# Kernel optimization log

Hardware: AMD Instinct MI355X
Metric: run time of the kernel (lower is better)

Reference implementation:

```python
import jax, jax.numpy as jnp
import numpy as np

BASE_T = 0.07
ALPHA = 0.5
EPS = 1e-12  # torch F.normalize eps


def _l2_normalize(x):
    norm = jnp.linalg.norm(x, axis=1, keepdims=True)
    return x / jnp.maximum(norm, EPS)


def setup_inputs() -> dict:
    key = jax.random.key(0)
    k1, k2, k3 = jax.random.split(key, 3)
    B, D, H, W = 4096, 512, 16, 16
    return {
        "emb1": jax.random.normal(k1, (B, D), dtype=jnp.float32),
        "emb2": jax.random.normal(k2, (B, D), dtype=jnp.float32),
        "attention_map": jax.random.uniform(k3, (B, H, W), dtype=jnp.float32),
    }


def reference(emb1, emb2, attention_map):
    B = emb1.shape[0]
    e1 = _l2_normalize(emb1)
    e2 = _l2_normalize(emb2)

    att = attention_map.mean(axis=(1, 2))                     # [B]
    temp = (BASE_T * (1.0 + ALPHA * att))[:, None]            # [B, 1]

    x = jnp.concatenate([e1, e2], axis=0)                     # [2B, D]
    x_swap = jnp.concatenate([e2, e1], axis=0)                # [2B, D]
    temp_cat = jnp.concatenate([temp, temp], axis=0)          # [2B, 1]

    sim = jnp.matmul(x, x.T) / temp_cat                       # [2B, 2B]
    pos_sim = jnp.sum(x * x_swap, axis=1) / temp_cat[:, 0]    # [2B]

    diag = jnp.eye(2 * B, dtype=bool)
    sim = jnp.where(diag, -jnp.inf, sim)                      # exp(-inf) = 0

    denominator = jnp.exp(sim).sum(axis=1)                    # [2B]
    loss = -jnp.log(jnp.exp(pos_sim) / denominator)
    return loss.mean()
```

## Files before the change

### kernel.cpp

```cpp
#include <hip/hip_runtime.h>
#include <hip/hip_bf16.h>
#include <math.h>

#define B_ROWS 4096
#define D_DIM 512
#define TWO_B 8192
#define HW_N 256
#define BASE_T 0.07f
#define ALPHA_C 0.5f
#define LOG2E 1.44269504088896340736f

typedef float v4f __attribute__((ext_vector_type(4)));

__device__ __forceinline__ float fast_exp2(float x) {
#if __has_builtin(__builtin_amdgcn_exp2f)
    return __builtin_amdgcn_exp2f(x);
#else
    return exp2f(x);
#endif
}

__global__ __launch_bounds__(256) void prep_kernel(
    const float* __restrict__ emb1, const float* __restrict__ emb2,
    const float* __restrict__ att, unsigned short* __restrict__ X8,
    float* __restrict__ inv_temp, float* __restrict__ pos)
{
    const int b = blockIdx.x;
    const int t = threadIdx.x;
    const float2 a1 = ((const float2*)(emb1 + (size_t)b * D_DIM))[t];
    const float2 a2 = ((const float2*)(emb2 + (size_t)b * D_DIM))[t];
    float av = att[(size_t)b * HW_N + t];
    float s1  = a1.x * a1.x + a1.y * a1.y;
    float s2  = a2.x * a2.x + a2.y * a2.y;
    float s12 = a1.x * a2.x + a1.y * a2.y;
    #pragma unroll
    for (int m = 1; m < 64; m <<= 1) {
        s1  += __shfl_xor(s1, m, 64);
        s2  += __shfl_xor(s2, m, 64);
        s12 += __shfl_xor(s12, m, 64);
        av  += __shfl_xor(av, m, 64);
    }
    __shared__ float red[4][4];
    const int w = t >> 6, lane = t & 63;
    if (lane == 0) { red[w][0] = s1; red[w][1] = s2; red[w][2] = s12; red[w][3] = av; }
    __syncthreads();
    const float T1  = red[0][0] + red[1][0] + red[2][0] + red[3][0];
    const float T2  = red[0][1] + red[1][1] + red[2][1] + red[3][1];
    const float T12 = red[0][2] + red[1][2] + red[2][2] + red[3][2];
    const float Ta  = red[0][3] + red[1][3] + red[2][3] + red[3][3];
    const float i1 = 1.0f / fmaxf(sqrtf(T1), 1e-12f);
    const float i2 = 1.0f / fmaxf(sqrtf(T2), 1e-12f);
    const float it = 1.0f / (BASE_T * (1.0f + ALPHA_C * (Ta * (1.0f / 256.0f))));
    const int p1 = __builtin_amdgcn_cvt_pk_fp8_f32(a1.x * i1, a1.y * i1, 0, false);
    const int p2 = __builtin_amdgcn_cvt_pk_fp8_f32(a2.x * i2, a2.y * i2, 0, false);
    X8[(size_t)b * 256 + t]            = (unsigned short)(p1 & 0xffff);
    X8[(size_t)(b + B_ROWS) * 256 + t] = (unsigned short)(p2 & 0xffff);
    if (t == 0) {
        inv_temp[b] = it * LOG2E;
        inv_temp[b + B_ROWS] = it * LOG2E;
        pos[b] = (T12 * i1 * i2) * it;
    }
}

__device__ __forceinline__ void gload_lds16(const void* g, void* s) {
    __builtin_amdgcn_global_load_lds(
        (const __attribute__((address_space(1))) unsigned int*)g,
        (__attribute__((address_space(3))) unsigned int*)s,
        16, 0, 0);
}

__global__ __launch_bounds__(256) void gram_kernel(
    const unsigned char* __restrict__ X8,
    const float* __restrict__ inv_temp,
    float* __restrict__ partial)
{
    const int bid = (blockIdx.x & 7) * 260 + (blockIdx.x >> 3);
    int rb = (int)((129.0f - sqrtf(129.0f * 129.0f - 8.0f * (float)bid)) * 0.5f);
    rb = rb < 0 ? 0 : (rb > 63 ? 63 : rb);
    while (rb > 0 && (rb * (129 - rb)) / 2 > bid) rb--;
    while (rb < 63 && ((rb + 1) * (129 - (rb + 1))) / 2 <= bid) rb++;
    const int cb = rb + (bid - (rb * (129 - rb)) / 2);

    __shared__ unsigned char smA[2][16384];
    __shared__ unsigned char smB[2][16384];

    const int rowBase = rb * 128;
    const int colBase = cb * 128;

    const int tid  = threadIdx.x;
    const int w    = tid >> 6;
    const int lane = tid & 63;
    const int quad = lane >> 4;
    const int t    = lane & 15;
    const int wm   = w >> 1;
    const int wn   = w & 1;

    const int srow   = lane >> 3;
    const int schunk = lane & 7;

    const unsigned char* Arow0 = X8 + (size_t)rowBase * D_DIM;
    const unsigned char* Brow0 = X8 + (size_t)colBase * D_DIM;

    v4f acc[4][4];
    #pragma unroll
    for (int a = 0; a < 4; a++)
        #pragma unroll
        for (int b2 = 0; b2 < 4; b2++)
            acc[a][b2] = v4f{0.0f, 0.0f, 0.0f, 0.0f};

    #pragma unroll
    for (int j = 0; j < 4; j++) {
        const int g = w * 4 + j;
        const int r = g * 8 + srow;
        const int gc = schunk ^ (r & 7);
        gload_lds16(Arow0 + (size_t)r * D_DIM + gc * 16, &smA[0][g * 1024]);
        gload_lds16(Brow0 + (size_t)r * D_DIM + gc * 16, &smB[0][g * 1024]);
    }
    __syncthreads();

    #pragma unroll
    for (int p = 0; p < 4; p++) {
        const int cur = p & 1;
        const int nxt = cur ^ 1;

        if (p < 3) {
            const int kk = (p + 1) * 128;
            #pragma unroll
            for (int j = 0; j < 4; j++) {
                const int g = w * 4 + j;
                const int r = g * 8 + srow;
                const int gc = schunk ^ (r & 7);
                gload_lds16(Arow0 + (size_t)r * D_DIM + kk + gc * 16, &smA[nxt][g * 1024]);
                gload_lds16(Brow0 + (size_t)r * D_DIM + kk + gc * 16, &smB[nxt][g * 1024]);
            }
        }

        #pragma unroll
        for (int s = 0; s < 4; s++) {
            const int pu = (s * 2 + (quad >> 1)) ^ (t & 7);
            const int off = pu * 16 + (quad & 1) * 8;
            long aF[4], bF[4];
            #pragma unroll
            for (int mi = 0; mi < 4; mi++)
                aF[mi] = *(const long*)&smA[cur][(wm * 64 + mi * 16 + t) * 128 + off];
            #pragma unroll
            for (int ni = 0; ni < 4; ni++)
                bF[ni] = *(const long*)&smB[cur][(wn * 64 + ni * 16 + t) * 128 + off];
            #pragma unroll
            for (int mi = 0; mi < 4; mi++)
                #pragma unroll
                for (int ni = 0; ni < 4; ni++)
                    acc[mi][ni] = __builtin_amdgcn_mfma_f32_16x16x32_fp8_fp8(
                        aF[mi], bF[ni], acc[mi][ni], 0, 0, 0);
        }

        __syncthreads();
    }

    v4f itv[4];
    #pragma unroll
    for (int mi = 0; mi < 4; mi++)
        itv[mi] = *(const v4f*)&inv_temp[rowBase + wm * 64 + mi * 16 + quad * 4];

    float* prow = partial + (size_t)(cb * 2 + wn) * TWO_B;
    #pragma unroll
    for (int mi = 0; mi < 4; mi++) {
        #pragma unroll
        for (int r = 0; r < 4; r++) {
            const int i = rowBase + wm * 64 + mi * 16 + quad * 4 + r;
            const float it = itv[mi][r];
            float s = 0.0f;
            #pragma unroll
            for (int ni = 0; ni < 4; ni++) {
                const int j = colBase + wn * 64 + ni * 16 + t;
                const float v = fast_exp2(acc[mi][ni][r] * it);
                s += (i == j) ? 0.0f : v;
            }
            s += __shfl_xor(s, 1, 64);
            s += __shfl_xor(s, 2, 64);
            s += __shfl_xor(s, 4, 64);
            s += __shfl_xor(s, 8, 64);
            if (t == 0) prow[i] = s;
        }
    }

    if (rb != cb) {
        float itj[4];
        float cs[4] = {0.0f, 0.0f, 0.0f, 0.0f};
        #pragma unroll
        for (int ni = 0; ni < 4; ni++)
            itj[ni] = inv_temp[colBase + wn * 64 + ni * 16 + t];
        #pragma unroll
        for (int mi = 0; mi < 4; mi++)
            #pragma unroll
            for (int r = 0; r < 4; r++)
                #pragma unroll
                for (int ni = 0; ni < 4; ni++)
                    cs[ni] += fast_exp2(acc[mi][ni][r] * itj[ni]);
        float* pcol = partial + (size_t)(rb * 2 + wm) * TWO_B;
        #pragma unroll
        for (int ni = 0; ni < 4; ni++) {
            cs[ni] += __shfl_xor(cs[ni], 16, 64);
            cs[ni] += __shfl_xor(cs[ni], 32, 64);
            if (quad == 0) pcol[colBase + wn * 64 + ni * 16 + t] = cs[ni];
        }
    }
}

__global__ __launch_bounds__(256) void finish1(
    const float* __restrict__ partial, const float* __restrict__ pos,
    float* __restrict__ blockSums)
{
    const int i = blockIdx.x * 256 + threadIdx.x;
    float d = 0.0f;
    #pragma unroll 8
    for (int s = 0; s < 128; s++) d += partial[(size_t)s * TWO_B + i];
    float li = logf(d) - pos[i & (B_ROWS - 1)];
    #pragma unroll
    for (int m = 1; m < 64; m <<= 1) li += __shfl_xor(li, m, 64);
    __shared__ float red[4];
    const int w = threadIdx.x >> 6, lane = threadIdx.x & 63;
    if (lane == 0) red[w] = li;
    __syncthreads();
    if (threadIdx.x == 0) blockSums[blockIdx.x] = red[0] + red[1] + red[2] + red[3];
}

__global__ void finish2(const float* __restrict__ blockSums, float* __restrict__ out)
{
    const int lane = threadIdx.x;
    float v = (lane < 32) ? blockSums[lane] : 0.0f;
    #pragma unroll
    for (int m = 1; m < 64; m <<= 1) v += __shfl_xor(v, m, 64);
    if (lane == 0) out[0] = v * (1.0f / 8192.0f);
}

extern "C" void kernel_launch(void* const* d_in, const int* in_sizes, int n_in,
                              void* d_out, int out_size, void* d_ws, size_t ws_size,
                              hipStream_t stream) {
    const float* emb1 = (const float*)d_in[0];
    const float* emb2 = (const float*)d_in[1];
    const float* att  = (const float*)d_in[2];
    float* out = (float*)d_out;

    char* ws = (char*)d_ws;
    unsigned short* X8 = (unsigned short*)ws;
    float* inv_temp    = (float*)(ws + 4194304);
    float* pos         = (float*)(ws + 4194304 + 32768);
    float* partial     = (float*)(ws + 4194304 + 32768 + 16384);
    float* blockSums   = (float*)(ws + 4194304 + 32768 + 16384 + 4194304);

    prep_kernel<<<B_ROWS, 256, 0, stream>>>(emb1, emb2, att, X8, inv_temp, pos);
    gram_kernel<<<2080, 256, 0, stream>>>((const unsigned char*)X8, inv_temp, partial);
    finish1<<<TWO_B / 256, 256, 0, stream>>>(partial, pos, blockSums);
    finish2<<<1, 64, 0, stream>>>(blockSums, out);
}
```

Measured before the change: 132.0 us.

## Use scaled 16x16x128 FP8 MFMA and load A fragments directly from global

Replaces the 16x16x32 FP8 MFMA with the gfx950 scaled 16x16x128 f8f6f4 MFMA (unit scales), cutting instruction count per k-step. The A operand is no longer staged through LDS: each lane reads its 32-byte fragment straight from global memory. This halves shared memory use, and a launch bound of 3 waves is added to raise occupancy. In exchange, A reads depend on global/L2 latency without double buffering, and the trailing sync on the last iteration is dropped.

```diff
diff --git a/kernel.cpp b/kernel.cpp
--- a/kernel.cpp
+++ b/kernel.cpp
@@ -11,6 +11,8 @@
 #define LOG2E 1.44269504088896340736f
 
 typedef float v4f __attribute__((ext_vector_type(4)));
+typedef int   v4i __attribute__((ext_vector_type(4)));
+typedef int   v8i __attribute__((ext_vector_type(8)));
 
 __device__ __forceinline__ float fast_exp2(float x) {
 #if __has_builtin(__builtin_amdgcn_exp2f)
@@ -69,7 +71,7 @@
         16, 0, 0);
 }
 
-__global__ __launch_bounds__(256) void gram_kernel(
+__global__ __launch_bounds__(256, 3) void gram_kernel(
     const unsigned char* __restrict__ X8,
     const float* __restrict__ inv_temp,
     float* __restrict__ partial)
@@ -81,7 +83,6 @@
     while (rb < 63 && ((rb + 1) * (129 - (rb + 1))) / 2 <= bid) rb++;
     const int cb = rb + (bid - (rb * (129 - rb)) / 2);
 
-    __shared__ unsigned char smA[2][16384];
     __shared__ unsigned char smB[2][16384];
 
     const int rowBase = rb * 128;
@@ -95,8 +96,8 @@
     const int wm   = w >> 1;
     const int wn   = w & 1;
 
-    const int srow   = lane >> 3;
-    const int schunk = lane & 7;
+    const int lr = lane >> 3;
+    const int su = (lane & 7) ^ lr;
 
     const unsigned char* Arow0 = X8 + (size_t)rowBase * D_DIM;
     const unsigned char* Brow0 = X8 + (size_t)colBase * D_DIM;
@@ -108,53 +109,60 @@
         for (int b2 = 0; b2 < 4; b2++)
             acc[a][b2] = v4f{0.0f, 0.0f, 0.0f, 0.0f};
 
+    const unsigned char* aPtr[4];
+    #pragma unroll
+    for (int mi = 0; mi < 4; mi++)
+        aPtr[mi] = Arow0 + (size_t)(wm * 64 + mi * 16 + t) * D_DIM + quad * 32;
+
+    const int r7 = t & 7;
+    const int bRow = (wn * 64 + t) * 128;
+
     #pragma unroll
     for (int j = 0; j < 4; j++) {
         const int g = w * 4 + j;
-        const int r = g * 8 + srow;
-        const int gc = schunk ^ (r & 7);
-        gload_lds16(Arow0 + (size_t)r * D_DIM + gc * 16, &smA[0][g * 1024]);
-        gload_lds16(Brow0 + (size_t)r * D_DIM + gc * 16, &smB[0][g * 1024]);
+        gload_lds16(Brow0 + (size_t)(g * 8 + lr) * D_DIM + su * 16,
+                    &smB[0][g * 1024]);
     }
     __syncthreads();
 
     #pragma unroll
     for (int p = 0; p < 4; p++) {
         const int cur = p & 1;
-        const int nxt = cur ^ 1;
+        const int kk  = p * 128;
 
         if (p < 3) {
-            const int kk = (p + 1) * 128;
+            const int kn = kk + 128;
             #pragma unroll
             for (int j = 0; j < 4; j++) {
                 const int g = w * 4 + j;
-                const int r = g * 8 + srow;
-                const int gc = schunk ^ (r & 7);
-                gload_lds16(Arow0 + (size_t)r * D_DIM + kk + gc * 16, &smA[nxt][g * 1024]);
-                gload_lds16(Brow0 + (size_t)r * D_DIM + kk + gc * 16, &smB[nxt][g * 1024]);
+                gload_lds16(Brow0 + (size_t)(g * 8 + lr) * D_DIM + kn + su * 16,
+                            &smB[cur ^ 1][g * 1024]);
             }
         }
 
-        #pragma unroll
-        for (int s = 0; s < 4; s++) {
-            const int pu = (s * 2 + (quad >> 1)) ^ (t & 7);
-            const int off = pu * 16 + (quad & 1) * 8;
-            long aF[4], bF[4];
+        v8i aF[4];
+        #pragma unroll
+        for (int mi = 0; mi < 4; mi++)
+            aF[mi] = *(const v8i*)(aPtr[mi] + kk);
+
+        #pragma unroll
+        for (int ni = 0; ni < 4; ni++) {
+            const unsigned char* rowp = &smB[cur][bRow + ni * 2048];
+            const int pu0 = (quad * 2) ^ r7;
+            const int pu1 = pu0 ^ 1;
+            v4i blo = *(const v4i*)(rowp + pu0 * 16);
+            v4i bhi = *(const v4i*)(rowp + pu1 * 16);
+            v8i bF = __builtin_shufflevector(blo, bhi, 0, 1, 2, 3, 4, 5, 6, 7);
             #pragma unroll
             for (int mi = 0; mi < 4; mi++)
-                aF[mi] = *(const long*)&smA[cur][(wm * 64 + mi * 16 + t) * 128 + off];
-            #pragma unroll
-            for (int ni = 0; ni < 4; ni++)
-                bF[ni] = *(const long*)&smB[cur][(wn * 64 + ni * 16 + t) * 128 + off];
-            #pragma unroll
-            for (int mi = 0; mi < 4; mi++)
-                #pragma unroll
-                for (int ni = 0; ni < 4; ni++)
-                    acc[mi][ni] = __builtin_amdgcn_mfma_f32_16x16x32_fp8_fp8(
-                        aF[mi], bF[ni], acc[mi][ni], 0, 0, 0);
-        }
-
-        __syncthreads();
+                acc[mi][ni] = __builtin_amdgcn_mfma_scale_f32_16x16x128_f8f6f4(
+                    aF[mi], bF, acc[mi][ni],
+                    0, 0,
+                    0, 0x7F7F7F7F,
+                    0, 0x7F7F7F7F);
+        }
+
+        if (p < 3) __syncthreads();
     }
 
     v4f itv[4];
```

Result: slower. 240.1 us (+81.8%).
